# Kernel tuning notes

Hardware: AMD Instinct MI355X
Metric: run time of the kernel (lower is better)

Reference implementation:

```python
import jax, jax.numpy as jnp
import numpy as np

N_NODES = 50000
N_EDGES = 800000
IN, HID, OUT = 256, 128, 64


def setup_inputs() -> dict:
    key = jax.random.key(0)
    ks = jax.random.split(key, 5)
    return {
        "x": jax.random.normal(ks[0], (N_NODES, IN), dtype=jnp.float32),
        "W1": jax.random.normal(ks[1], (IN, HID), dtype=jnp.float32) / np.sqrt(IN),
        "b1": jnp.zeros((HID,), dtype=jnp.float32),
        "W2": jax.random.normal(ks[2], (HID, OUT), dtype=jnp.float32) / np.sqrt(HID),
        "b2": jnp.zeros((OUT,), dtype=jnp.float32),
        "src": jax.random.randint(ks[3], (N_EDGES,), 0, N_NODES, dtype=jnp.int32),
        "dst": jax.random.randint(ks[4], (N_EDGES,), 0, N_NODES, dtype=jnp.int32),
    }


def _graph_conv(h, W, b, src, dst, norm_src, norm_dst, n_nodes):
    # DGL GraphConv, norm='both': y = D_dst^{-1/2} A D_src^{-1/2} h W + b
    # Project first (smaller feature dim for the SpMM), linearity makes it exact.
    h = h @ W                                     # [N, d_out]
    msg = (h * norm_src[:, None])[src]            # gather per-edge   [E, d_out]
    agg = jax.ops.segment_sum(msg, dst, num_segments=n_nodes)  # [N, d_out]
    return agg * norm_dst[:, None] + b


def reference(x, W1, b1, W2, b2, src, dst):
    n = x.shape[0]
    ones = jnp.ones(src.shape[0], dtype=jnp.float32)
    out_deg = jnp.zeros(n, jnp.float32).at[src].add(ones)
    in_deg = jnp.zeros(n, jnp.float32).at[dst].add(ones)
    norm_src = jax.lax.rsqrt(jnp.maximum(out_deg, 1.0))
    norm_dst = jax.lax.rsqrt(jnp.maximum(in_deg, 1.0))

    h = _graph_conv(x, W1, b1, src, dst, norm_src, norm_dst, n)
    h = jax.nn.relu(h)
    return _graph_conv(h, W2, b2, src, dst, norm_src, norm_dst, n)
```

## Files before the change

kernel.cpp:

```cpp
#include <hip/hip_runtime.h>

#define NN 50000
#define NE 800000
#define NPAD 50176
#define NSLICE 32
#define ESL 25000
#define HPN 25088
#define HPW 12544
#define FPN 12544
#define GB 782
#define NB 196

typedef __attribute__((ext_vector_type(8))) short bf16x8;
typedef __attribute__((ext_vector_type(4))) float f32x4;

__device__ __forceinline__ float u2f(unsigned u) { return __uint_as_float(u); }
__device__ __forceinline__ unsigned f2u(float f) { return __float_as_uint(f); }
__device__ __forceinline__ unsigned short f2bf(float f) {
    unsigned u = f2u(f);
    return (unsigned short)((u + (((u >> 16) & 1u) + 0x7fffu)) >> 16);
}

__global__ __launch_bounds__(1024) void hist_wtrans_kernel(
    const int* __restrict__ src, const int* __restrict__ dst,
    unsigned* __restrict__ cnt_sl,
    const float* __restrict__ W1, const float* __restrict__ W2,
    unsigned short* __restrict__ Wh1, unsigned short* __restrict__ Wl1,
    unsigned short* __restrict__ Wh2, unsigned short* __restrict__ Wl2,
    int* __restrict__ done_cnt) {
    if (blockIdx.x == 0 && threadIdx.x == 0) *done_cnt = 0;
    const int b = blockIdx.x;
    if (b >= 128) {
        float w;
        unsigned short *ph, *pl;
        int f;
        if (b < 160) {
            int i = (b - 128) * 1024 + threadIdx.x;
            int k = i >> 7, n = i & 127;
            f = (((n >> 4) * 32 + (k >> 3)) * 16 + (n & 15)) * 8 + (k & 7);
            w = W1[i]; ph = Wh1; pl = Wl1;
        } else {
            int i = (b - 160) * 1024 + threadIdx.x;
            int k = i >> 6, n = i & 63;
            f = (((n >> 4) * 16 + (k >> 3)) * 16 + (n & 15)) * 8 + (k & 7);
            w = W2[i]; ph = Wh2; pl = Wl2;
        }
        unsigned u = f2u(w);
        float lo = w - u2f(u & 0xffff0000u);
        ph[f] = (unsigned short)(u >> 16);
        pl[f] = (unsigned short)(f2u(lo) >> 16);
        return;
    }
    __shared__ unsigned lcnt[HPW];
    const int side = b & 1;
    const int slice = (b >> 1) & (NSLICE - 1);
    const int part = b >> 6;
    const int* __restrict__ arr = side ? dst : src;
    const int base = part * HPN;
    for (int j = threadIdx.x; j < HPW; j += 1024) lcnt[j] = 0;
    __syncthreads();
    const int e0 = slice * ESL;
    for (int i = e0 + threadIdx.x; i < e0 + ESL; i += 1024) {
        int v = arr[i] - base;
        if ((unsigned)v < (unsigned)HPN)
            atomicAdd(&lcnt[v >> 1], 1u << ((v & 1) * 16));
    }
    __syncthreads();
    unsigned* o = cnt_sl + (size_t)b * HPW;
    for (int j = threadIdx.x; j < HPW; j += 1024) o[j] = lcnt[j];
}

__global__ __launch_bounds__(256) void norm_scanAB_kernel(
    const unsigned* __restrict__ cnt_sl, float* __restrict__ ns,
    float* __restrict__ nd, int* __restrict__ presum,
    int* __restrict__ pref, int* __restrict__ blk_sum,
    int* __restrict__ blk_ofs, int* __restrict__ done_cnt, int n) {
    __shared__ int lds[256];
    __shared__ int is_last;
    int i = blockIdx.x * 256 + threadIdx.x;
    int d_total = 0;
    if (i < n) {
        int part = (i >= HPN) ? 1 : 0;
        int w = (i - part * HPN) >> 1;
        int sh = (i & 1) * 16;
        int s_total = 0;
#pragma unroll
        for (int sl = 0; sl < NSLICE; sl++) {
            int bb = part * 64 + sl * 2;
            s_total += (cnt_sl[(size_t)bb * HPW + w] >> sh) & 0xffff;
            int c = (cnt_sl[(size_t)(bb + 1) * HPW + w] >> sh) & 0xffff;
            presum[sl * NPAD + i] = d_total;
            d_total += c;
        }
        ns[i] = rsqrtf(fmaxf((float)s_total, 1.0f));
        nd[i] = rsqrtf(fmaxf((float)d_total, 1.0f));
    }
    lds[threadIdx.x] = d_total;
    __syncthreads();
    for (int ofs = 1; ofs < 256; ofs <<= 1) {
        int t = (threadIdx.x >= ofs) ? lds[threadIdx.x - ofs] : 0;
        __syncthreads();
        lds[threadIdx.x] += t;
        __syncthreads();
    }
    if (i < n) pref[i] = lds[threadIdx.x] - d_total;
    if (threadIdx.x == 255) blk_sum[blockIdx.x] = lds[255];
    __threadfence();
    if (threadIdx.x == 0) {
        int c = atomicAdd(done_cnt, 1);
        is_last = (c == gridDim.x - 1);
    }
    __syncthreads();
    if (!is_last) return;
    __threadfence();
    int v = (threadIdx.x < gridDim.x) ? blk_sum[threadIdx.x] : 0;
    __syncthreads();
    lds[threadIdx.x] = v;
    __syncthreads();
    for (int ofs = 1; ofs < 256; ofs <<= 1) {
        int t = (threadIdx.x >= ofs) ? lds[threadIdx.x - ofs] : 0;
        __syncthreads();
        lds[threadIdx.x] += t;
        __syncthreads();
    }
    if (threadIdx.x < gridDim.x) blk_ofs[threadIdx.x] = lds[threadIdx.x] - v;
}

__global__ __launch_bounds__(1024) void fill_kernel(
    const int* __restrict__ src, const int* __restrict__ dst,
    const int* __restrict__ pref, const int* __restrict__ blk_ofs,
    const int* __restrict__ presum, int* __restrict__ eidx) {
    __shared__ int cur[FPN];
    const int slice = blockIdx.x >> 2;
    const int part = blockIdx.x & 3;
    const int base = part * FPN;
    for (int j = threadIdx.x; j < FPN; j += 1024) {
        int gi = base + j;
        cur[j] = (gi < NN) ? pref[gi] + blk_ofs[gi >> 8] + presum[slice * NPAD + gi] : 0;
    }
    __syncthreads();
    const int e0 = slice * ESL;
    for (int i = e0 + threadIdx.x; i < e0 + ESL; i += 1024) {
        int v = dst[i] - base;
        if ((unsigned)v < (unsigned)FPN) {
            int pos = atomicAdd(&cur[v], 1);
            eidx[pos] = src[i];
        }
    }
}

__global__ __launch_bounds__(256) void gemm1_kernel(
    const float* __restrict__ A, const unsigned short* __restrict__ Wh,
    const unsigned short* __restrict__ Wl, const float* __restrict__ norm_src,
    unsigned short* __restrict__ out, int M) {
    constexpr int N = 128, K = 256;
    constexpr int NT = N / 16, KC = K / 32;
    const int wave = threadIdx.x >> 6;
    const int lane = threadIdx.x & 63;
    const int ln = lane & 15;
    const int qk = lane >> 4;
    const int m0 = blockIdx.x * 64 + wave * 16;
    const int mA = m0 + ln;
    const float* Arow = A + (size_t)(mA < M ? mA : (M - 1)) * K + qk * 8;
    const bf16x8* BH = (const bf16x8*)Wh;
    const bf16x8* BL = (const bf16x8*)Wl;

    f32x4 acc[NT];
#pragma unroll
    for (int t = 0; t < NT; t++) acc[t] = (f32x4){0.f, 0.f, 0.f, 0.f};

#pragma unroll 2
    for (int c = 0; c < KC; ++c) {
        float4 a0 = *(const float4*)(Arow + c * 32);
        float4 a1 = *(const float4*)(Arow + c * 32 + 4);
        float av[8] = {a0.x, a0.y, a0.z, a0.w, a1.x, a1.y, a1.z, a1.w};
        bf16x8 ah, al;
#pragma unroll
        for (int j = 0; j < 8; ++j) {
            unsigned u = f2u(av[j]);
            float lo = av[j] - u2f(u & 0xffff0000u);
            ah[j] = (short)(u >> 16);
            al[j] = (short)(f2u(lo) >> 16);
        }
        const int fb = c * 4 + qk;
#pragma unroll
        for (int t = 0; t < NT; ++t) {
            bf16x8 bh = BH[(t * (K / 8) + fb) * 16 + ln];
            bf16x8 bl = BL[(t * (K / 8) + fb) * 16 + ln];
            acc[t] = __builtin_amdgcn_mfma_f32_16x16x32_bf16(ah, bh, acc[t], 0, 0, 0);
            acc[t] = __builtin_amdgcn_mfma_f32_16x16x32_bf16(ah, bl, acc[t], 0, 0, 0);
            acc[t] = __builtin_amdgcn_mfma_f32_16x16x32_bf16(al, bh, acc[t], 0, 0, 0);
        }
    }
    float sc[4];
#pragma unroll
    for (int r = 0; r < 4; ++r) {
        int row = m0 + qk * 4 + r;
        sc[r] = (row < M) ? norm_src[row] : 0.f;
    }
#pragma unroll
    for (int t = 0; t < NT; ++t)
#pragma unroll
        for (int r = 0; r < 4; ++r) {
            int row = m0 + qk * 4 + r;
            if (row < M) out[(size_t)row * N + t * 16 + ln] = f2bf(acc[t][r] * sc[r]);
        }
}

__global__ __launch_bounds__(256) void layer2_kernel(
    const unsigned* __restrict__ hs1, const int* __restrict__ eidx,
    const int* __restrict__ pref, const int* __restrict__ blk_ofs,
    const float* __restrict__ norm_src, const float* __restrict__ norm_dst,
    const float* __restrict__ bias, const unsigned short* __restrict__ Wh,
    const unsigned short* __restrict__ Wl, unsigned short* __restrict__ hs2, int n) {
    __shared__ unsigned lh1[16 * 68];
    const int wave = threadIdx.x >> 6;
    const int lane = threadIdx.x & 63;
    const int nb = blockIdx.x * 16;

    for (int j = 0; j < 4; ++j) {
        const int node = nb + wave * 4 + j;
        float rx = 0.f, ry = 0.f;
        if (node < n) {
            int beg = pref[node] + blk_ofs[node >> 8];
            int end = (node + 1 < n) ? pref[node + 1] + blk_ofs[(node + 1) >> 8] : NE;
            float ax = 0.f, ay = 0.f;
            int e = beg;
            for (; e + 7 < end; e += 8) {
                unsigned u0 = hs1[(size_t)eidx[e] * 64 + lane];
                unsigned u1 = hs1[(size_t)eidx[e + 1] * 64 + lane];
                unsigned u2 = hs1[(size_t)eidx[e + 2] * 64 + lane];
                unsigned u3 = hs1[(size_t)eidx[e + 3] * 64 + lane];
                unsigned u4 = hs1[(size_t)eidx[e + 4] * 64 + lane];
                unsigned u5 = hs1[(size_t)eidx[e + 5] * 64 + lane];
                unsigned u6 = hs1[(size_t)eidx[e + 6] * 64 + lane];
                unsigned u7 = hs1[(size_t)eidx[e + 7] * 64 + lane];
                ax += u2f(u0 << 16) + u2f(u1 << 16) + u2f(u2 << 16) + u2f(u3 << 16) +
                      u2f(u4 << 16) + u2f(u5 << 16) + u2f(u6 << 16) + u2f(u7 << 16);
                ay += u2f(u0 & 0xffff0000u) + u2f(u1 & 0xffff0000u) +
                      u2f(u2 & 0xffff0000u) + u2f(u3 & 0xffff0000u) +
                      u2f(u4 & 0xffff0000u) + u2f(u5 & 0xffff0000u) +
                      u2f(u6 & 0xffff0000u) + u2f(u7 & 0xffff0000u);
            }
            for (; e + 3 < end; e += 4) {
                unsigned u0 = hs1[(size_t)eidx[e] * 64 + lane];
                unsigned u1 = hs1[(size_t)eidx[e + 1] * 64 + lane];
                unsigned u2 = hs1[(size_t)eidx[e + 2] * 64 + lane];
                unsigned u3 = hs1[(size_t)eidx[e + 3] * 64 + lane];
                ax += u2f(u0 << 16) + u2f(u1 << 16) + u2f(u2 << 16) + u2f(u3 << 16);
                ay += u2f(u0 & 0xffff0000u) + u2f(u1 & 0xffff0000u) +
                      u2f(u2 & 0xffff0000u) + u2f(u3 & 0xffff0000u);
            }
            for (; e < end; ++e) {
                unsigned u0 = hs1[(size_t)eidx[e] * 64 + lane];
                ax += u2f(u0 << 16);
                ay += u2f(u0 & 0xffff0000u);
            }
            float sc = norm_dst[node];
            float2 b = ((const float2*)bias)[lane];
            rx = fmaxf(ax * sc + b.x, 0.f);
            ry = fmaxf(ay * sc + b.y, 0.f);
        }
        lh1[(wave * 4 + j) * 68 + lane] = (unsigned)f2bf(rx) | ((unsigned)f2bf(ry) << 16);
    }
    __syncthreads();

    const int ln = lane & 15;
    const int qk = lane >> 4;
    const int t = wave;
    const bf16x8* BH = (const bf16x8*)Wh;
    const bf16x8* BL = (const bf16x8*)Wl;
    f32x4 acc = (f32x4){0.f, 0.f, 0.f, 0.f};
#pragma unroll
    for (int c = 0; c < 4; ++c) {
        bf16x8 ah = *(const bf16x8*)&lh1[ln * 68 + c * 16 + qk * 4];
        const int fb = c * 4 + qk;
        bf16x8 bh = BH[(t * 16 + fb) * 16 + ln];
        bf16x8 bl = BL[(t * 16 + fb) * 16 + ln];
        acc = __builtin_amdgcn_mfma_f32_16x16x32_bf16(ah, bh, acc, 0, 0, 0);
        acc = __builtin_amdgcn_mfma_f32_16x16x32_bf16(ah, bl, acc, 0, 0, 0);
    }
#pragma unroll
    for (int r = 0; r < 4; ++r) {
        int node = nb + qk * 4 + r;
        if (node < n)
            hs2[(size_t)node * 64 + t * 16 + ln] = f2bf(acc[r] * norm_src[node]);
    }
}

__global__ __launch_bounds__(256) void gather64_kernel(
    const unsigned* __restrict__ hs, const int* __restrict__ eidx,
    const int* __restrict__ pref, const int* __restrict__ blk_ofs,
    const float* __restrict__ norm_dst, const float* __restrict__ bias,
    float* __restrict__ out, int n) {
    int wave = (blockIdx.x * blockDim.x + threadIdx.x) >> 6;
    int lane = threadIdx.x & 63;
    if (wave >= n) return;
    int beg = pref[wave] + blk_ofs[wave >> 8];
    int end = (wave + 1 < n) ? pref[wave + 1] + blk_ofs[(wave + 1) >> 8] : NE;
    int half = lane >> 5;
    int dim = lane & 31;
    float ax = 0.f, ay = 0.f;
    int e = beg + half;
    for (; e + 6 < end; e += 8) {
        unsigned u0 = hs[(size_t)eidx[e] * 32 + dim];
        unsigned u1 = hs[(size_t)eidx[e + 2] * 32 + dim];
        unsigned u2 = hs[(size_t)eidx[e + 4] * 32 + dim];
        unsigned u3 = hs[(size_t)eidx[e + 6] * 32 + dim];
        ax += u2f(u0 << 16) + u2f(u1 << 16) + u2f(u2 << 16) + u2f(u3 << 16);
        ay += u2f(u0 & 0xffff0000u) + u2f(u1 & 0xffff0000u) +
              u2f(u2 & 0xffff0000u) + u2f(u3 & 0xffff0000u);
    }
    for (; e < end; e += 2) {
        unsigned u0 = hs[(size_t)eidx[e] * 32 + dim];
        ax += u2f(u0 << 16);
        ay += u2f(u0 & 0xffff0000u);
    }
    ax += __shfl_xor(ax, 32);
    ay += __shfl_xor(ay, 32);
    if (half == 0) {
        float sc = norm_dst[wave];
        float2 b = ((const float2*)bias)[dim];
        ((float2*)out)[(size_t)wave * 32 + dim] =
            make_float2(ax * sc + b.x, ay * sc + b.y);
    }
}

extern "C" void kernel_launch(void* const* d_in, const int* in_sizes, int n_in,
                              void* d_out, int out_size, void* d_ws, size_t ws_size,
                              hipStream_t stream) {
    const float* x  = (const float*)d_in[0];
    const float* W1 = (const float*)d_in[1];
    const float* b1 = (const float*)d_in[2];
    const float* W2 = (const float*)d_in[3];
    const float* b2 = (const float*)d_in[4];
    const int* src  = (const int*)d_in[5];
    const int* dst  = (const int*)d_in[6];
    float* out = (float*)d_out;
    char* ws = (char*)d_ws;

    float* norm_src = (float*)(ws);
    float* norm_dst = (float*)(ws + 4 * 50176);
    int*   pref     = (int*)(ws + 4 * 100352);
    int*   blk_sum  = (int*)(ws + 4 * 150528);
    int*   blk_ofs  = (int*)(ws + 4 * 150784);
    int*   done_cnt = (int*)(ws + 4 * 151040);
    int*   eidx     = (int*)(ws + 4 * 151296);
    unsigned short* Wh1 = (unsigned short*)(ws + 4 * 951296);
    unsigned short* Wl1 = (unsigned short*)(ws + 4 * 967680);
    unsigned short* Wh2 = (unsigned short*)(ws + 4 * 984064);
    unsigned short* Wl2 = (unsigned short*)(ws + 4 * 988160);
    unsigned short* hs1 = (unsigned short*)(ws + 4 * 992256);
    unsigned short* hs2 = (unsigned short*)(ws + 4 * 4192256);
    unsigned* cnt_sl    = (unsigned*)(ws + 4 * 5792256);
    int* presum         = (int*)(ws + 4 * 7397888);

    hist_wtrans_kernel<<<168, 1024, 0, stream>>>(src, dst, cnt_sl, W1, W2,
                                                 Wh1, Wl1, Wh2, Wl2, done_cnt);

    norm_scanAB_kernel<<<NB, 256, 0, stream>>>(cnt_sl, norm_src, norm_dst,
                                               presum, pref, blk_sum, blk_ofs,
                                               done_cnt, NN);

    gemm1_kernel<<<GB, 256, 0, stream>>>(x, Wh1, Wl1, norm_src, hs1, NN);

    fill_kernel<<<128, 1024, 0, stream>>>(src, dst, pref, blk_ofs, presum, eidx);

    layer2_kernel<<<3125, 256, 0, stream>>>(
        (const unsigned*)hs1, eidx, pref, blk_ofs, norm_src, norm_dst, b1,
        Wh2, Wl2, hs2, NN);

    gather64_kernel<<<12500, 256, 0, stream>>>(
        (const unsigned*)hs2, eidx, pref, blk_ofs, norm_dst, b2, out, NN);
}
```

Measured before the change: 239.7 us.

## Merge GEMM1 with CSR fill and vectorize neighbor gathers to 16-byte loads

Folds the independent layer-1 GEMM and the CSR fill into one launch with 512-thread blocks, so both run side by side and one launch is dropped. The layer-2 and output gathers now have each lane load a uint4 (8 bf16 values) and process several edges per wave at once, then combine the partial sums with cross-lane shuffles. The aim is fewer, wider memory transactions and more edges in flight. In exchange it adds shuffle reductions and masked tail handling, and the merged kernel must use 512 threads and the fill's 50KB of shared memory for the GEMM blocks as well, which may reduce occupancy.

```diff
diff --git a/kernel.cpp b/kernel.cpp
--- a/kernel.cpp
+++ b/kernel.cpp
@@ -8,7 +8,8 @@
 #define HPN 25088
 #define HPW 12544
 #define FPN 12544
-#define GB 782
+#define GB2 391
+#define FB 128
 #define NB 196
 
 typedef __attribute__((ext_vector_type(8))) short bf16x8;
@@ -19,6 +20,12 @@
 __device__ __forceinline__ unsigned short f2bf(float f) {
     unsigned u = f2u(f);
     return (unsigned short)((u + (((u >> 16) & 1u) + 0x7fffu)) >> 16);
+}
+__device__ __forceinline__ void acc8(float* ax, uint4 u) {
+    ax[0] += u2f(u.x << 16); ax[1] += u2f(u.x & 0xffff0000u);
+    ax[2] += u2f(u.y << 16); ax[3] += u2f(u.y & 0xffff0000u);
+    ax[4] += u2f(u.z << 16); ax[5] += u2f(u.z & 0xffff0000u);
+    ax[6] += u2f(u.w << 16); ax[7] += u2f(u.w & 0xffff0000u);
 }
 
 __global__ __launch_bounds__(1024) void hist_wtrans_kernel(
@@ -126,85 +133,87 @@
     if (threadIdx.x < gridDim.x) blk_ofs[threadIdx.x] = lds[threadIdx.x] - v;
 }
 
-__global__ __launch_bounds__(1024) void fill_kernel(
+__global__ __launch_bounds__(512) void gemm1_fill_kernel(
+    const float* __restrict__ A, const unsigned short* __restrict__ Wh,
+    const unsigned short* __restrict__ Wl, const float* __restrict__ norm_src,
+    unsigned short* __restrict__ out,
     const int* __restrict__ src, const int* __restrict__ dst,
     const int* __restrict__ pref, const int* __restrict__ blk_ofs,
-    const int* __restrict__ presum, int* __restrict__ eidx) {
+    const int* __restrict__ presum, int* __restrict__ eidx, int M) {
     __shared__ int cur[FPN];
-    const int slice = blockIdx.x >> 2;
-    const int part = blockIdx.x & 3;
+    const int b = blockIdx.x;
+    if (b < GB2) {
+        constexpr int N = 128, K = 256;
+        constexpr int NT = N / 16, KC = K / 32;
+        const int wave = threadIdx.x >> 6;
+        const int lane = threadIdx.x & 63;
+        const int ln = lane & 15;
+        const int qk = lane >> 4;
+        const int m0 = b * 128 + wave * 16;
+        const int mA = m0 + ln;
+        const float* Arow = A + (size_t)(mA < M ? mA : (M - 1)) * K + qk * 8;
+        const bf16x8* BH = (const bf16x8*)Wh;
+        const bf16x8* BL = (const bf16x8*)Wl;
+
+        f32x4 acc[NT];
+#pragma unroll
+        for (int t = 0; t < NT; t++) acc[t] = (f32x4){0.f, 0.f, 0.f, 0.f};
+
+#pragma unroll 2
+        for (int c = 0; c < KC; ++c) {
+            float4 a0 = *(const float4*)(Arow + c * 32);
+            float4 a1 = *(const float4*)(Arow + c * 32 + 4);
+            float av[8] = {a0.x, a0.y, a0.z, a0.w, a1.x, a1.y, a1.z, a1.w};
+            bf16x8 ah, al;
+#pragma unroll
+            for (int j = 0; j < 8; ++j) {
+                unsigned u = f2u(av[j]);
+                float lo = av[j] - u2f(u & 0xffff0000u);
+                ah[j] = (short)(u >> 16);
+                al[j] = (short)(f2u(lo) >> 16);
+            }
+            const int fb = c * 4 + qk;
+#pragma unroll
+            for (int t = 0; t < NT; ++t) {
+                bf16x8 bh = BH[(t * (K / 8) + fb) * 16 + ln];
+                bf16x8 bl = BL[(t * (K / 8) + fb) * 16 + ln];
+                acc[t] = __builtin_amdgcn_mfma_f32_16x16x32_bf16(ah, bh, acc[t], 0, 0, 0);
+                acc[t] = __builtin_amdgcn_mfma_f32_16x16x32_bf16(ah, bl, acc[t], 0, 0, 0);
+                acc[t] = __builtin_amdgcn_mfma_f32_16x16x32_bf16(al, bh, acc[t], 0, 0, 0);
+            }
+        }
+        float sc[4];
+#pragma unroll
+        for (int r = 0; r < 4; ++r) {
+            int row = m0 + qk * 4 + r;
+            sc[r] = (row < M) ? norm_src[row] : 0.f;
+        }
+#pragma unroll
+        for (int t = 0; t < NT; ++t)
+#pragma unroll
+            for (int r = 0; r < 4; ++r) {
+                int row = m0 + qk * 4 + r;
+                if (row < M) out[(size_t)row * N + t * 16 + ln] = f2bf(acc[t][r] * sc[r]);
+            }
+        return;
+    }
+    const int fb = b - GB2;
+    const int slice = fb >> 2;
+    const int part = fb & 3;
     const int base = part * FPN;
-    for (int j = threadIdx.x; j < FPN; j += 1024) {
+    for (int j = threadIdx.x; j < FPN; j += 512) {
         int gi = base + j;
         cur[j] = (gi < NN) ? pref[gi] + blk_ofs[gi >> 8] + presum[slice * NPAD + gi] : 0;
     }
     __syncthreads();
     const int e0 = slice * ESL;
-    for (int i = e0 + threadIdx.x; i < e0 + ESL; i += 1024) {
+    for (int i = e0 + threadIdx.x; i < e0 + ESL; i += 512) {
         int v = dst[i] - base;
         if ((unsigned)v < (unsigned)FPN) {
             int pos = atomicAdd(&cur[v], 1);
             eidx[pos] = src[i];
         }
     }
-}
-
-__global__ __launch_bounds__(256) void gemm1_kernel(
-    const float* __restrict__ A, const unsigned short* __restrict__ Wh,
-    const unsigned short* __restrict__ Wl, const float* __restrict__ norm_src,
-    unsigned short* __restrict__ out, int M) {
-    constexpr int N = 128, K = 256;
-    constexpr int NT = N / 16, KC = K / 32;
-    const int wave = threadIdx.x >> 6;
-    const int lane = threadIdx.x & 63;
-    const int ln = lane & 15;
-    const int qk = lane >> 4;
-    const int m0 = blockIdx.x * 64 + wave * 16;
-    const int mA = m0 + ln;
-    const float* Arow = A + (size_t)(mA < M ? mA : (M - 1)) * K + qk * 8;
-    const bf16x8* BH = (const bf16x8*)Wh;
-    const bf16x8* BL = (const bf16x8*)Wl;
-
-    f32x4 acc[NT];
-#pragma unroll
-    for (int t = 0; t < NT; t++) acc[t] = (f32x4){0.f, 0.f, 0.f, 0.f};
-
-#pragma unroll 2
-    for (int c = 0; c < KC; ++c) {
-        float4 a0 = *(const float4*)(Arow + c * 32);
-        float4 a1 = *(const float4*)(Arow + c * 32 + 4);
-        float av[8] = {a0.x, a0.y, a0.z, a0.w, a1.x, a1.y, a1.z, a1.w};
-        bf16x8 ah, al;
-#pragma unroll
-        for (int j = 0; j < 8; ++j) {
-            unsigned u = f2u(av[j]);
-            float lo = av[j] - u2f(u & 0xffff0000u);
-            ah[j] = (short)(u >> 16);
-            al[j] = (short)(f2u(lo) >> 16);
-        }
-        const int fb = c * 4 + qk;
-#pragma unroll
-        for (int t = 0; t < NT; ++t) {
-            bf16x8 bh = BH[(t * (K / 8) + fb) * 16 + ln];
-            bf16x8 bl = BL[(t * (K / 8) + fb) * 16 + ln];
-            acc[t] = __builtin_amdgcn_mfma_f32_16x16x32_bf16(ah, bh, acc[t], 0, 0, 0);
-            acc[t] = __builtin_amdgcn_mfma_f32_16x16x32_bf16(ah, bl, acc[t], 0, 0, 0);
-            acc[t] = __builtin_amdgcn_mfma_f32_16x16x32_bf16(al, bh, acc[t], 0, 0, 0);
-        }
-    }
-    float sc[4];
-#pragma unroll
-    for (int r = 0; r < 4; ++r) {
-        int row = m0 + qk * 4 + r;
-        sc[r] = (row < M) ? norm_src[row] : 0.f;
-    }
-#pragma unroll
-    for (int t = 0; t < NT; ++t)
-#pragma unroll
-        for (int r = 0; r < 4; ++r) {
-            int row = m0 + qk * 4 + r;
-            if (row < M) out[(size_t)row * N + t * 16 + ln] = f2bf(acc[t][r] * sc[r]);
-        }
 }
 
 __global__ __launch_bounds__(256) void layer2_kernel(
@@ -217,51 +226,52 @@
     const int wave = threadIdx.x >> 6;
     const int lane = threadIdx.x & 63;
     const int nb = blockIdx.x * 16;
+    const int q = lane >> 4;
+    const int p = lane & 15;
 
     for (int j = 0; j < 4; ++j) {
         const int node = nb + wave * 4 + j;
-        float rx = 0.f, ry = 0.f;
+        float ax[8];
+#pragma unroll
+        for (int k = 0; k < 8; ++k) ax[k] = 0.f;
+        unsigned pk[4] = {0u, 0u, 0u, 0u};
         if (node < n) {
             int beg = pref[node] + blk_ofs[node >> 8];
             int end = (node + 1 < n) ? pref[node + 1] + blk_ofs[(node + 1) >> 8] : NE;
-            float ax = 0.f, ay = 0.f;
             int e = beg;
             for (; e + 7 < end; e += 8) {
-                unsigned u0 = hs1[(size_t)eidx[e] * 64 + lane];
-                unsigned u1 = hs1[(size_t)eidx[e + 1] * 64 + lane];
-                unsigned u2 = hs1[(size_t)eidx[e + 2] * 64 + lane];
-                unsigned u3 = hs1[(size_t)eidx[e + 3] * 64 + lane];
-                unsigned u4 = hs1[(size_t)eidx[e + 4] * 64 + lane];
-                unsigned u5 = hs1[(size_t)eidx[e + 5] * 64 + lane];
-                unsigned u6 = hs1[(size_t)eidx[e + 6] * 64 + lane];
-                unsigned u7 = hs1[(size_t)eidx[e + 7] * 64 + lane];
-                ax += u2f(u0 << 16) + u2f(u1 << 16) + u2f(u2 << 16) + u2f(u3 << 16) +
-                      u2f(u4 << 16) + u2f(u5 << 16) + u2f(u6 << 16) + u2f(u7 << 16);
-                ay += u2f(u0 & 0xffff0000u) + u2f(u1 & 0xffff0000u) +
-                      u2f(u2 & 0xffff0000u) + u2f(u3 & 0xffff0000u) +
-                      u2f(u4 & 0xffff0000u) + u2f(u5 & 0xffff0000u) +
-                      u2f(u6 & 0xffff0000u) + u2f(u7 & 0xffff0000u);
-            }
-            for (; e + 3 < end; e += 4) {
-                unsigned u0 = hs1[(size_t)eidx[e] * 64 + lane];
-                unsigned u1 = hs1[(size_t)eidx[e + 1] * 64 + lane];
-                unsigned u2 = hs1[(size_t)eidx[e + 2] * 64 + lane];
-                unsigned u3 = hs1[(size_t)eidx[e + 3] * 64 + lane];
-                ax += u2f(u0 << 16) + u2f(u1 << 16) + u2f(u2 << 16) + u2f(u3 << 16);
-                ay += u2f(u0 & 0xffff0000u) + u2f(u1 & 0xffff0000u) +
-                      u2f(u2 & 0xffff0000u) + u2f(u3 & 0xffff0000u);
-            }
-            for (; e < end; ++e) {
-                unsigned u0 = hs1[(size_t)eidx[e] * 64 + lane];
-                ax += u2f(u0 << 16);
-                ay += u2f(u0 & 0xffff0000u);
+                int i0 = eidx[e + q];
+                int i1 = eidx[e + 4 + q];
+                uint4 u0 = *(const uint4*)(hs1 + (size_t)i0 * 64 + p * 4);
+                uint4 u1 = *(const uint4*)(hs1 + (size_t)i1 * 64 + p * 4);
+                acc8(ax, u0);
+                acc8(ax, u1);
+            }
+            for (; e < end; e += 4) {
+                int ee = e + q;
+                bool ok = ee < end;
+                int i0 = eidx[ok ? ee : beg];
+                uint4 u0 = *(const uint4*)(hs1 + (size_t)i0 * 64 + p * 4);
+                if (ok) acc8(ax, u0);
+            }
+#pragma unroll
+            for (int k = 0; k < 8; ++k) {
+                ax[k] += __shfl_xor(ax[k], 16);
+                ax[k] += __shfl_xor(ax[k], 32);
             }
             float sc = norm_dst[node];
-            float2 b = ((const float2*)bias)[lane];
-            rx = fmaxf(ax * sc + b.x, 0.f);
-            ry = fmaxf(ay * sc + b.y, 0.f);
-        }
-        lh1[(wave * 4 + j) * 68 + lane] = (unsigned)f2bf(rx) | ((unsigned)f2bf(ry) << 16);
+            float4 b0 = *(const float4*)(bias + p * 8);
+            float4 b1 = *(const float4*)(bias + p * 8 + 4);
+            float bb[8] = {b0.x, b0.y, b0.z, b0.w, b1.x, b1.y, b1.z, b1.w};
+#pragma unroll
+            for (int k = 0; k < 4; ++k) {
+                float rlo = fmaxf(ax[2 * k] * sc + bb[2 * k], 0.f);
+                float rhi = fmaxf(ax[2 * k + 1] * sc + bb[2 * k + 1], 0.f);
+                pk[k] = (unsigned)f2bf(rlo) | ((unsigned)f2bf(rhi) << 16);
+            }
+        }
+        if (q == 0)
+            *(uint4*)&lh1[(wave * 4 + j) * 68 + p * 4] = *(uint4*)pk;
     }
     __syncthreads();
 
@@ -298,31 +308,48 @@
     if (wave >= n) return;
     int beg = pref[wave] + blk_ofs[wave >> 8];
     int end = (wave + 1 < n) ? pref[wave + 1] + blk_ofs[(wave + 1) >> 8] : NE;
-    int half = lane >> 5;
-    int dim = lane & 31;
-    float ax = 0.f, ay = 0.f;
-    int e = beg + half;
-    for (; e + 6 < end; e += 8) {
-        unsigned u0 = hs[(size_t)eidx[e] * 32 + dim];
-        unsigned u1 = hs[(size_t)eidx[e + 2] * 32 + dim];
-        unsigned u2 = hs[(size_t)eidx[e + 4] * 32 + dim];
-        unsigned u3 = hs[(size_t)eidx[e + 6] * 32 + dim];
-        ax += u2f(u0 << 16) + u2f(u1 << 16) + u2f(u2 << 16) + u2f(u3 << 16);
-        ay += u2f(u0 & 0xffff0000u) + u2f(u1 & 0xffff0000u) +
-              u2f(u2 & 0xffff0000u) + u2f(u3 & 0xffff0000u);
-    }
-    for (; e < end; e += 2) {
-        unsigned u0 = hs[(size_t)eidx[e] * 32 + dim];
-        ax += u2f(u0 << 16);
-        ay += u2f(u0 & 0xffff0000u);
-    }
-    ax += __shfl_xor(ax, 32);
-    ay += __shfl_xor(ay, 32);
-    if (half == 0) {
+    const int o = lane >> 3;
+    const int p = lane & 7;
+    float ax[8];
+#pragma unroll
+    for (int k = 0; k < 8; ++k) ax[k] = 0.f;
+    int e = beg;
+    for (; e + 15 < end; e += 16) {
+        int i0 = eidx[e + o];
+        int i1 = eidx[e + 8 + o];
+        uint4 u0 = *(const uint4*)(hs + (size_t)i0 * 32 + p * 4);
+        uint4 u1 = *(const uint4*)(hs + (size_t)i1 * 32 + p * 4);
+        acc8(ax, u0);
+        acc8(ax, u1);
+    }
+    for (; e < end; e += 8) {
+        int ee = e + o;
+        bool ok = ee < end;
+        int i0 = eidx[ok ? ee : beg];
+        uint4 u0 = *(const uint4*)(hs + (size_t)i0 * 32 + p * 4);
+        if (ok) acc8(ax, u0);
+    }
+#pragma unroll
+    for (int k = 0; k < 8; ++k) {
+        ax[k] += __shfl_xor(ax[k], 8);
+        ax[k] += __shfl_xor(ax[k], 16);
+        ax[k] += __shfl_xor(ax[k], 32);
+    }
+    if (o == 0) {
         float sc = norm_dst[wave];
-        float2 b = ((const float2*)bias)[dim];
-        ((float2*)out)[(size_t)wave * 32 + dim] =
-            make_float2(ax * sc + b.x, ay * sc + b.y);
+        float4 b0 = *(const float4*)(bias + p * 8);
+        float4 b1 = *(const float4*)(bias + p * 8 + 4);
+        float4 r0, r1;
+        r0.x = ax[0] * sc + b0.x;
+        r0.y = ax[1] * sc + b0.y;
+        r0.z = ax[2] * sc + b0.z;
+        r0.w = ax[3] * sc + b0.w;
+        r1.x = ax[4] * sc + b1.x;
+        r1.y = ax[5] * sc + b1.y;
+        r1.z = ax[6] * sc + b1.z;
+        r1.w = ax[7] * sc + b1.w;
+        *(float4*)(out + (size_t)wave * 64 + p * 8) = r0;
+        *(float4*)(out + (size_t)wave * 64 + p * 8 + 4) = r1;
     }
 }
 
@@ -362,9 +389,8 @@
                                                presum, pref, blk_sum, blk_ofs,
                                                done_cnt, NN);
 
-    gemm1_kernel<<<GB, 256, 0, stream>>>(x, Wh1, Wl1, norm_src, hs1, NN);
-
-    fill_kernel<<<128, 1024, 0, stream>>>(src, dst, pref, blk_ofs, presum, eidx);
+    gemm1_fill_kernel<<<GB2 + FB, 512, 0, stream>>>(
+        x, Wh1, Wl1, norm_src, hs1, src, dst, pref, blk_ofs, presum, eidx, NN);
 
     layer2_kernel<<<3125, 256, 0, stream>>>(
         (const unsigned*)hs1, eidx, pref, blk_ofs, norm_src, norm_dst, b1,
```

Result: no change. 240.2 us (+0.2%).
